# Kernel tuning notes

Measured on AMD Instinct MI355X. Metric: run time of the kernel, lower is better.

The kernel has to match this reference:

```python
import jax, jax.numpy as jnp
import numpy as np

N, E, D, H, O, L = 50000, 400000, 128, 128, 64, 2


def setup_inputs() -> dict:
    key = jax.random.key(0)
    ks = jax.random.split(key, 24)
    s = 0.05
    rn = lambda k, shape: jax.random.normal(k, shape, jnp.float32) * s
    # random edges with no self-loops (dst = src + nonzero offset mod N)
    src = jax.random.randint(ks[0], (E,), 0, N, dtype=jnp.int32)
    off = jax.random.randint(ks[1], (E,), 1, N, dtype=jnp.int32)
    dst = (src + off) % N
    edge_index = jnp.stack([src, dst])  # [2, E] int32
    return {
        "x": rn(ks[2], (N, D)),
        "edge_index": edge_index,
        "attn_W": rn(ks[3], (L, 2 * D, 2)),
        "attn_b": rn(ks[4], (L, 2)),
        "mlp_W1": rn(ks[5], (L, D, H)),
        "mlp_b1": rn(ks[6], (L, H)),
        "mlp_W2": rn(ks[7], (L, H, H)),
        "mlp_b2": rn(ks[8], (L, H)),
        "bn_gamma": jnp.ones((L, H), jnp.float32),   # torch BatchNorm1d default affine init
        "bn_beta": jnp.zeros((L, H), jnp.float32),
        "gru_Wih": rn(ks[9], (D, 3 * H)),
        "gru_Whh": rn(ks[10], (H, 3 * H)),
        "gru_bih": rn(ks[11], (3 * H,)),
        "gru_bhh": rn(ks[12], (3 * H,)),
        "last_W1": rn(ks[13], (H, H)),
        "last_b1": rn(ks[14], (H,)),
        "last_W2": rn(ks[15], (H, O)),
        "last_b2": rn(ks[16], (O,)),
    }


def reference(x, edge_index, attn_W, attn_b, mlp_W1, mlp_b1, mlp_W2, mlp_b2,
              bn_gamma, bn_beta, gru_Wih, gru_Whh, gru_bih, gru_bhh,
              last_W1, last_b1, last_W2, last_b2):
    n = x.shape[0]
    # symmetrize edge list: message (nbr -> node) for both directions
    node = jnp.concatenate([edge_index[0], edge_index[1]])  # destination
    nbr = jnp.concatenate([edge_index[1], edge_index[0]])   # source / neighbor
    deg = jax.ops.segment_sum(jnp.ones((node.shape[0], 1), x.dtype), node, num_segments=n)
    has_nbr = deg > 0

    h_state = jnp.zeros((n, gru_Whh.shape[0]), x.dtype)
    for l in range(attn_W.shape[0]):
        feats = x[nbr]  # [2E, d] gather
        s_agg = jax.ops.segment_sum(feats, node, num_segments=n)
        m_agg = jax.ops.segment_max(feats, node, num_segments=n)
        m_agg = jnp.where(has_nbr, m_agg, jnp.zeros_like(m_agg))  # isolated nodes stay 0
        # attention over {sum, max} aggregations
        scores = jnp.concatenate([s_agg, m_agg], axis=1) @ attn_W[l] + attn_b[l]  # [n, 2]
        w = jax.nn.softmax(scores, axis=1)
        comb = x + w[:, :1] * s_agg + w[:, 1:] * m_agg
        # MLP (in -> hidden, ReLU, hidden -> out)
        z = jax.nn.relu(comb @ mlp_W1[l] + mlp_b1[l]) @ mlp_W2[l] + mlp_b2[l]
        # BatchNorm1d in eval mode with running stats (mean 0, var 1): affine only
        z = z * bn_gamma[l] + bn_beta[l]
        # GRUCell
        gi = z @ gru_Wih + gru_bih
        gh = h_state @ gru_Whh + gru_bhh
        ir, iz, inn = jnp.split(gi, 3, axis=1)
        hr, hz, hn = jnp.split(gh, 3, axis=1)
        r = jax.nn.sigmoid(ir + hr)
        u = jax.nn.sigmoid(iz + hz)
        ncand = jnp.tanh(inn + r * hn)
        h_state = (1.0 - u) * ncand + u * h_state
        x = h_state
    # final node-level MLP
    out = jax.nn.relu(x @ last_W1 + last_b1) @ last_W2 + last_b2
    return out
```

## Files before the change

### kernel.cpp

```cpp
#include <hip/hip_runtime.h>
#include <math.h>

typedef unsigned short u16;
typedef __attribute__((ext_vector_type(8))) short bf16x8;
typedef __attribute__((ext_vector_type(4))) float f32x4;

__device__ __forceinline__ u16 f2b(float f) {
    union { float f; unsigned u; } v; v.f = f;
    unsigned r = (v.u + 0x7FFF + ((v.u >> 16) & 1)) >> 16;
    return (u16)r;
}
__device__ __forceinline__ float b2f(u16 h) {
    union { unsigned u; float f; } v; v.u = (unsigned)h << 16;
    return v.f;
}
__device__ __forceinline__ float fsig(float x) { return 1.f / (1.f + __expf(-x)); }
__device__ __forceinline__ float ftanh(float x) {
    float e = __expf(2.f * x);
    return 1.f - 2.f / (e + 1.f);
}

__device__ __forceinline__ void gll16(const void* g, void* l) {
    __builtin_amdgcn_global_load_lds(
        (const __attribute__((address_space(1))) void*)g,
        (__attribute__((address_space(3))) void*)l, 16, 0, 0);
}

template <int BYTES>
__device__ __forceinline__ void stage_lin(const u16* g, u16* l, int wid, int lane) {
#pragma unroll
    for (int i = 0; i < BYTES / 8192; ++i) {
        int off = (i * 8 + wid) * 1024;
        gll16((const char*)g + off + lane * 16, (char*)l + off);
    }
}

__global__ void k_deg(const int* __restrict__ ei, int* __restrict__ cnt, int E) {
    int e = blockIdx.x * 256 + threadIdx.x;
    if (e < E) {
        atomicAdd(&cnt[ei[e]], 1);
        atomicAdd(&cnt[ei[E + e]], 1);
    }
}

__global__ __launch_bounds__(1024) void k_scan_sum(const int* __restrict__ cnt,
                                                   int* __restrict__ part, int N) {
    __shared__ int sd[16];
    int t = threadIdx.x;
    int i = blockIdx.x * 1024 + t;
    int v = (i < N) ? cnt[i] : 0;
#pragma unroll
    for (int o = 32; o; o >>= 1) v += __shfl_xor(v, o);
    if ((t & 63) == 0) sd[t >> 6] = v;
    __syncthreads();
    if (t < 16) {
        int s = sd[t];
#pragma unroll
        for (int o = 8; o; o >>= 1) s += __shfl_xor(s, o);
        if (t == 0) part[blockIdx.x] = s;
    }
}

__global__ void k_scan_part(int* __restrict__ part, int nb) {
    int t = threadIdx.x;
    int v = (t < nb) ? part[t] : 0;
#pragma unroll
    for (int o = 1; o < 64; o <<= 1) {
        int u = __shfl_up(v, o);
        if ((t & 63) >= o) v += u;
    }
    if (t < nb) part[t] = v;
}

__global__ __launch_bounds__(1024) void k_scan_write(const int* __restrict__ cnt,
                                                     const int* __restrict__ part,
                                                     int* __restrict__ offs, int N) {
    __shared__ int sd[16];
    int t = threadIdx.x, lane = t & 63, wid = t >> 6;
    int i = blockIdx.x * 1024 + t;
    int v = (i < N) ? cnt[i] : 0;
    int inc = v;
#pragma unroll
    for (int o = 1; o < 64; o <<= 1) {
        int u = __shfl_up(inc, o);
        if (lane >= o) inc += u;
    }
    if (lane == 63) sd[wid] = inc;
    __syncthreads();
    if (wid == 0) {
        int wv = (lane < 16) ? sd[lane] : 0;
#pragma unroll
        for (int o = 1; o < 16; o <<= 1) {
            int u = __shfl_up(wv, o);
            if (lane >= o) wv += u;
        }
        if (lane < 16) sd[lane] = wv;
    }
    __syncthreads();
    int base = (blockIdx.x > 0 ? part[blockIdx.x - 1] : 0) + (wid > 0 ? sd[wid - 1] : 0);
    if (i < N) offs[i + 1] = base + inc;
    if (i == 0 && blockIdx.x == 0) offs[0] = 0;
}

__global__ void k_fill(const int* __restrict__ ei, int* __restrict__ cur,
                       u16* __restrict__ adj, int E) {
    int e = blockIdx.x * 256 + threadIdx.x;
    if (e < E) {
        int s = ei[e], d = ei[E + e];
        int p = atomicAdd(&cur[s], 1); adj[p] = (u16)d;
        int q = atomicAdd(&cur[d], 1); adj[q] = (u16)s;
    }
}

__device__ __forceinline__ void conv_chunk(const float* __restrict__ src,
                                           u16* __restrict__ dst, int c, int NC) {
    int sl = c / NC, n = c - sl * NC;
    u16 tmp[8];
#pragma unroll
    for (int i = 0; i < 8; ++i) tmp[i] = f2b(src[(size_t)(sl * 8 + i) * NC + n]);
    *(uint4*)(dst + (size_t)c * 8) = *(const uint4*)tmp;
}

__global__ void k_prep_w(const float* __restrict__ W1, const float* __restrict__ W2,
                         const float* __restrict__ Wih, const float* __restrict__ Whh,
                         const float* __restrict__ lW1, const float* __restrict__ lW2,
                         u16* __restrict__ tW1, u16* __restrict__ tW2,
                         u16* __restrict__ tGRU,
                         u16* __restrict__ tlW1, u16* __restrict__ tlW2, int L) {
    int c = blockIdx.x * 256 + threadIdx.x;
    if (c < L * 2048) { int l = c >> 11; conv_chunk(W1 + (size_t)l * 16384, tW1 + (size_t)l * 16384, c & 2047, 128); return; }
    c -= L * 2048;
    if (c < L * 2048) { int l = c >> 11; conv_chunk(W2 + (size_t)l * 16384, tW2 + (size_t)l * 16384, c & 2047, 128); return; }
    c -= L * 2048;
    if (c < 12288) {
        int s = c / 1536, r = c % 1536;
        int q = r / 384, r2 = r % 384;
        int mat = r2 / 192, cc = r2 % 192;
        int h = s >> 2, kc = s & 3;
        int tt = cc >> 4, ii = cc & 15;
        int g = tt >> 2;
        int ocol = g * 128 + h * 64 + (tt & 3) * 16 + ii;
        const float* src = mat ? Whh : Wih;
        int kb = (kc * 4 + q) * 8;
        u16 tmp[8];
#pragma unroll
        for (int e = 0; e < 8; ++e) tmp[e] = f2b(src[(size_t)(kb + e) * 384 + ocol]);
        *(uint4*)(tGRU + (size_t)c * 8) = *(const uint4*)tmp;
        return;
    }
    c -= 12288;
    if (c < 2048) { conv_chunk(lW1, tlW1, c, 128); return; }
    c -= 2048;
    if (c < 1024) { conv_chunk(lW2, tlW2, c, 64); return; }
}

__global__ void k_f2b(const float* __restrict__ src, u16* __restrict__ dst, int n8) {
    int i = blockIdx.x * 256 + threadIdx.x;
    if (i < n8) {
        float4 a = *(const float4*)(src + (size_t)i * 8);
        float4 b = *(const float4*)(src + (size_t)i * 8 + 4);
        u16 t[8] = {f2b(a.x), f2b(a.y), f2b(a.z), f2b(a.w),
                    f2b(b.x), f2b(b.y), f2b(b.z), f2b(b.w)};
        *(uint4*)(dst + (size_t)i * 8) = *(const uint4*)t;
    }
}

__global__ __launch_bounds__(256) void k_agg(const u16* __restrict__ xb,
                                             const u16* __restrict__ adj,
                                             const int* __restrict__ offs,
                                             const float* __restrict__ aW,
                                             const float* __restrict__ ab,
                                             u16* __restrict__ comb, int N) {
    int n = blockIdx.x * 4 + (threadIdx.x >> 6);
    if (n >= N) return;
    int l = threadIdx.x & 63;
    int half = l >> 5, e0 = (l & 31) * 4;
    int beg = offs[n], end = offs[n + 1];
    float s0 = 0.f, s1 = 0.f, s2 = 0.f, s3 = 0.f;
    float m0 = -3.402823e38f, m1 = m0, m2 = m0, m3 = m0;
    int j = beg + half;
    for (; j + 6 < end; j += 8) {
        int a0 = adj[j], a1 = adj[j + 2], a2 = adj[j + 4], a3 = adj[j + 6];
        ushort4 v0 = *(const ushort4*)(xb + (size_t)a0 * 128 + e0);
        ushort4 v1 = *(const ushort4*)(xb + (size_t)a1 * 128 + e0);
        ushort4 v2 = *(const ushort4*)(xb + (size_t)a2 * 128 + e0);
        ushort4 v3 = *(const ushort4*)(xb + (size_t)a3 * 128 + e0);
        float f0, f1, f2, f3;
        f0 = b2f(v0.x); f1 = b2f(v0.y); f2 = b2f(v0.z); f3 = b2f(v0.w);
        s0 += f0; s1 += f1; s2 += f2; s3 += f3;
        m0 = fmaxf(m0, f0); m1 = fmaxf(m1, f1); m2 = fmaxf(m2, f2); m3 = fmaxf(m3, f3);
        f0 = b2f(v1.x); f1 = b2f(v1.y); f2 = b2f(v1.z); f3 = b2f(v1.w);
        s0 += f0; s1 += f1; s2 += f2; s3 += f3;
        m0 = fmaxf(m0, f0); m1 = fmaxf(m1, f1); m2 = fmaxf(m2, f2); m3 = fmaxf(m3, f3);
        f0 = b2f(v2.x); f1 = b2f(v2.y); f2 = b2f(v2.z); f3 = b2f(v2.w);
        s0 += f0; s1 += f1; s2 += f2; s3 += f3;
        m0 = fmaxf(m0, f0); m1 = fmaxf(m1, f1); m2 = fmaxf(m2, f2); m3 = fmaxf(m3, f3);
        f0 = b2f(v3.x); f1 = b2f(v3.y); f2 = b2f(v3.z); f3 = b2f(v3.w);
        s0 += f0; s1 += f1; s2 += f2; s3 += f3;
        m0 = fmaxf(m0, f0); m1 = fmaxf(m1, f1); m2 = fmaxf(m2, f2); m3 = fmaxf(m3, f3);
    }
    for (; j < end; j += 2) {
        int nb = adj[j];
        ushort4 v = *(const ushort4*)(xb + (size_t)nb * 128 + e0);
        float f0 = b2f(v.x), f1 = b2f(v.y), f2 = b2f(v.z), f3 = b2f(v.w);
        s0 += f0; s1 += f1; s2 += f2; s3 += f3;
        m0 = fmaxf(m0, f0); m1 = fmaxf(m1, f1); m2 = fmaxf(m2, f2); m3 = fmaxf(m3, f3);
    }
    s0 += __shfl_xor(s0, 32); m0 = fmaxf(m0, __shfl_xor(m0, 32));
    s1 += __shfl_xor(s1, 32); m1 = fmaxf(m1, __shfl_xor(m1, 32));
    s2 += __shfl_xor(s2, 32); m2 = fmaxf(m2, __shfl_xor(m2, 32));
    s3 += __shfl_xor(s3, 32); m3 = fmaxf(m3, __shfl_xor(m3, 32));
    if (beg == end) { m0 = m1 = m2 = m3 = 0.f; }
    float p0 = 0.f, p1 = 0.f;
    {
        float2 w0v = *(const float2*)(aW + (size_t)e0 * 2);
        float2 w1v = *(const float2*)(aW + (size_t)(e0 + 1) * 2);
        float2 w2v = *(const float2*)(aW + (size_t)(e0 + 2) * 2);
        float2 w3v = *(const float2*)(aW + (size_t)(e0 + 3) * 2);
        float2 u0v = *(const float2*)(aW + (size_t)(128 + e0) * 2);
        float2 u1v = *(const float2*)(aW + (size_t)(128 + e0 + 1) * 2);
        float2 u2v = *(const float2*)(aW + (size_t)(128 + e0 + 2) * 2);
        float2 u3v = *(const float2*)(aW + (size_t)(128 + e0 + 3) * 2);
        p0 = s0 * w0v.x + s1 * w1v.x + s2 * w2v.x + s3 * w3v.x
           + m0 * u0v.x + m1 * u1v.x + m2 * u2v.x + m3 * u3v.x;
        p1 = s0 * w0v.y + s1 * w1v.y + s2 * w2v.y + s3 * w3v.y
           + m0 * u0v.y + m1 * u1v.y + m2 * u2v.y + m3 * u3v.y;
    }
#pragma unroll
    for (int o = 16; o; o >>= 1) { p0 += __shfl_xor(p0, o); p1 += __shfl_xor(p1, o); }
    p0 += ab[0]; p1 += ab[1];
    float pm = fmaxf(p0, p1);
    float ea = __expf(p0 - pm), eb = __expf(p1 - pm);
    float w0 = ea / (ea + eb), w1 = 1.f - w0;
    if (half == 0) {
        ushort4 xv = *(const ushort4*)(xb + (size_t)n * 128 + e0);
        ushort4 o;
        o.x = f2b(b2f(xv.x) + w0 * s0 + w1 * m0);
        o.y = f2b(b2f(xv.y) + w0 * s1 + w1 * m1);
        o.z = f2b(b2f(xv.z) + w0 * s2 + w1 * m2);
        o.w = f2b(b2f(xv.w) + w0 * s3 + w1 * m3);
        *(ushort4*)(comb + (size_t)n * 128 + e0) = o;
    }
}

template <bool H0, bool WF32>
__global__ __launch_bounds__(512, 4) void k_layer(
    const u16* __restrict__ Cb, const u16* __restrict__ Hb,
    const float* __restrict__ Hf,
    const u16* __restrict__ W1t, const float* __restrict__ b1,
    const u16* __restrict__ W2t, const float* __restrict__ b2,
    const float* __restrict__ gam, const float* __restrict__ bet,
    const u16* __restrict__ tG,
    const float* __restrict__ bih, const float* __restrict__ bhh,
    float* __restrict__ HnF, u16* __restrict__ HnB, int M) {
    __shared__ __align__(16) u16 x_s[128 * 16 * 8];
    __shared__ __align__(16) u16 b_s[2][12288];
    const int t = threadIdx.x;
    const int m0 = blockIdx.x * 128;
    const int wid = t >> 6, lane = t & 63, lo = lane & 15, hi = lane >> 4;
    const int w = wid;
    const int arow = 16 * w + lo;

#pragma unroll
    for (int i = 0; i < 4; ++i) {
        int off = (i * 8 + wid) * 1024;
        int row = (off >> 8) + (lane >> 4);
        int s = lane & 15;
        int gr = m0 + row; gr = gr < M ? gr : M - 1;
        gll16(Cb + (size_t)gr * 128 + ((s ^ (row & 7)) * 8), (char*)x_s + off);
    }
    bf16x8 hreg[4];
    if (!H0) {
        int gr = m0 + arow; gr = gr < M ? gr : M - 1;
#pragma unroll
        for (int kc = 0; kc < 4; ++kc)
            hreg[kc] = *(const bf16x8*)(Hb + (size_t)gr * 128 + (kc * 4 + hi) * 8);
    }
    stage_lin<16384>(W1t, b_s[0], wid, lane);
    stage_lin<16384>(W1t + 8192, b_s[1], wid, lane);
    __syncthreads();

    f32x4 acc[8];
#pragma unroll
    for (int j = 0; j < 8; ++j) acc[j] = (f32x4)0.f;
#pragma unroll
    for (int ks = 0; ks < 4; ++ks) {
        bf16x8 af = *(const bf16x8*)&x_s[(arow * 16 + ((ks * 4 + hi) ^ (arow & 7))) * 8];
        const u16* wb = b_s[ks >> 1];
        int loc = (ks & 1) * 4 + hi;
#pragma unroll
        for (int j = 0; j < 8; ++j) {
            bf16x8 bf = *(const bf16x8*)&wb[((size_t)loc * 128 + 16 * j + lo) * 8];
            acc[j] = __builtin_amdgcn_mfma_f32_16x16x32_bf16(af, bf, acc[j], 0, 0, 0);
        }
    }
    __syncthreads();
    stage_lin<16384>(W2t, b_s[0], wid, lane);
    stage_lin<16384>(W2t + 8192, b_s[1], wid, lane);
#pragma unroll
    for (int j = 0; j < 8; ++j) {
        int c = 16 * j + lo;
        float bv = b1[c];
#pragma unroll
        for (int q = 0; q < 4; ++q) {
            int row = 16 * w + hi * 4 + q;
            float v = fmaxf(acc[j][q] + bv, 0.f);
            int sl = c >> 3;
            x_s[(row * 16 + (sl ^ (row & 7))) * 8 + (c & 7)] = f2b(v);
        }
    }
    __syncthreads();

#pragma unroll
    for (int j = 0; j < 8; ++j) acc[j] = (f32x4)0.f;
#pragma unroll
    for (int ks = 0; ks < 4; ++ks) {
        bf16x8 af = *(const bf16x8*)&x_s[(arow * 16 + ((ks * 4 + hi) ^ (arow & 7))) * 8];
        const u16* wb = b_s[ks >> 1];
        int loc = (ks & 1) * 4 + hi;
#pragma unroll
        for (int j = 0; j < 8; ++j) {
            bf16x8 bf = *(const bf16x8*)&wb[((size_t)loc * 128 + 16 * j + lo) * 8];
            acc[j] = __builtin_amdgcn_mfma_f32_16x16x32_bf16(af, bf, acc[j], 0, 0, 0);
        }
    }
    __syncthreads();
    stage_lin<24576>(tG, b_s[0], wid, lane);
    stage_lin<24576>(tG + 12288, b_s[1], wid, lane);
#pragma unroll
    for (int j = 0; j < 8; ++j) {
        int c = 16 * j + lo;
        float bv = b2[c], gv = gam[c], tv = bet[c];
#pragma unroll
        for (int q = 0; q < 4; ++q) {
            int row = 16 * w + hi * 4 + q;
            float v = (acc[j][q] + bv) * gv + tv;
            int sl = c >> 3;
            x_s[(row * 16 + (sl ^ (row & 7))) * 8 + (c & 7)] = f2b(v);
        }
    }
    __syncthreads();

    f32x4 racc[4], uacc[4], nza[4], nha[4];

    auto gru_kc = [&](const u16* buf, int kc) {
        bf16x8 zf = *(const bf16x8*)&x_s[(arow * 16 + ((kc * 4 + hi) ^ (arow & 7))) * 8];
#pragma unroll
        for (int jj = 0; jj < 4; ++jj) {
            const u16* bi = &buf[((size_t)(hi * 2 + 0) * 192) * 8];
            bf16x8 wr = *(const bf16x8*)&bi[(jj * 16 + lo) * 8];
            racc[jj] = __builtin_amdgcn_mfma_f32_16x16x32_bf16(zf, wr, racc[jj], 0, 0, 0);
            bf16x8 wu = *(const bf16x8*)&bi[(64 + jj * 16 + lo) * 8];
            uacc[jj] = __builtin_amdgcn_mfma_f32_16x16x32_bf16(zf, wu, uacc[jj], 0, 0, 0);
            bf16x8 wn = *(const bf16x8*)&bi[(128 + jj * 16 + lo) * 8];
            nza[jj] = __builtin_amdgcn_mfma_f32_16x16x32_bf16(zf, wn, nza[jj], 0, 0, 0);
            if (!H0) {
                const u16* bh = &buf[((size_t)(hi * 2 + 1) * 192) * 8];
                bf16x8 vr = *(const bf16x8*)&bh[(jj * 16 + lo) * 8];
                racc[jj] = __builtin_amdgcn_mfma_f32_16x16x32_bf16(hreg[kc], vr, racc[jj], 0, 0, 0);
                bf16x8 vu = *(const bf16x8*)&bh[(64 + jj * 16 + lo) * 8];
                uacc[jj] = __builtin_amdgcn_mfma_f32_16x16x32_bf16(hreg[kc], vu, uacc[jj], 0, 0, 0);
                bf16x8 vn = *(const bf16x8*)&bh[(128 + jj * 16 + lo) * 8];
                nha[jj] = __builtin_amdgcn_mfma_f32_16x16x32_bf16(hreg[kc], vn, nha[jj], 0, 0, 0);
            }
        }
    };

    auto gru_epi = [&](int h) {
#pragma unroll
        for (int ct = 0; ct < 4; ++ct) {
            int c = h * 64 + ct * 16 + lo;
            float b_r = bih[c] + bhh[c];
            float b_u = bih[c + 128] + bhh[c + 128];
            float b_in = bih[c + 256], b_hn = bhh[c + 256];
#pragma unroll
            for (int q = 0; q < 4; ++q) {
                int r = m0 + 16 * w + hi * 4 + q;
                if (r < M) {
                    float rr = fsig(racc[ct][q] + b_r);
                    float uu = fsig(uacc[ct][q] + b_u);
                    float hterm = H0 ? b_hn : (nha[ct][q] + b_hn);
                    float nn = ftanh(nza[ct][q] + b_in + rr * hterm);
                    float hv = H0 ? 0.f : Hf[(size_t)r * 128 + c];
                    float o = (1.f - uu) * nn + uu * hv;
                    if (WF32) HnF[(size_t)r * 128 + c] = o;
                    HnB[(size_t)r * 128 + c] = f2b(o);
                }
            }
        }
    };

#pragma unroll
    for (int j = 0; j < 4; ++j) { racc[j] = (f32x4)0.f; uacc[j] = (f32x4)0.f;
                                  nza[j] = (f32x4)0.f; nha[j] = (f32x4)0.f; }
    gru_kc(b_s[0], 0);
    gru_kc(b_s[1], 1);
    __syncthreads();
    stage_lin<24576>(tG + 2 * 12288, b_s[0], wid, lane);
    stage_lin<24576>(tG + 3 * 12288, b_s[1], wid, lane);
    __syncthreads();
    gru_kc(b_s[0], 2);
    gru_kc(b_s[1], 3);
    __syncthreads();
    stage_lin<24576>(tG + 4 * 12288, b_s[0], wid, lane);
    stage_lin<24576>(tG + 5 * 12288, b_s[1], wid, lane);
    gru_epi(0);
    __syncthreads();

#pragma unroll
    for (int j = 0; j < 4; ++j) { racc[j] = (f32x4)0.f; uacc[j] = (f32x4)0.f;
                                  nza[j] = (f32x4)0.f; nha[j] = (f32x4)0.f; }
    gru_kc(b_s[0], 0);
    gru_kc(b_s[1], 1);
    __syncthreads();
    stage_lin<24576>(tG + 6 * 12288, b_s[0], wid, lane);
    stage_lin<24576>(tG + 7 * 12288, b_s[1], wid, lane);
    __syncthreads();
    gru_kc(b_s[0], 2);
    gru_kc(b_s[1], 3);
    gru_epi(1);
}

__global__ __launch_bounds__(256, 2) void k_final(const u16* __restrict__ Hb,
                                                  const u16* __restrict__ W1t,
                                                  const float* __restrict__ b1,
                                                  const u16* __restrict__ W2t,
                                                  const float* __restrict__ b2,
                                                  float* __restrict__ out, int M) {
    __shared__ __align__(16) u16 x_s[64 * 16 * 8];
    __shared__ __align__(16) u16 w_s[16 * 128 * 8];
    const int t = threadIdx.x;
    const int m0 = blockIdx.x * 64;
    const int w = t >> 6, l = t & 63, lo = l & 15, hi = l >> 4;
    const int arow = 16 * w + lo;
#pragma unroll
    for (int i = 0; i < 4; ++i) {
        int idx = t + i * 256;
        int row = idx >> 4, sl = idx & 15;
        int gr = m0 + row; gr = gr < M ? gr : M - 1;
        *(uint4*)&x_s[(row * 16 + (sl ^ (row & 7))) * 8] =
            *(const uint4*)(Hb + (size_t)gr * 128 + sl * 8);
    }
#pragma unroll
    for (int i = 0; i < 8; ++i) {
        int idx = t + i * 256;
        *(uint4*)&w_s[idx * 8] = *(const uint4*)(W1t + (size_t)idx * 8);
    }
    __syncthreads();
    f32x4 acc[8];
#pragma unroll
    for (int j = 0; j < 8; ++j) acc[j] = (f32x4)0.f;
#pragma unroll
    for (int ks = 0; ks < 4; ++ks) {
        bf16x8 af = *(const bf16x8*)&x_s[(arow * 16 + ((ks * 4 + hi) ^ (arow & 7))) * 8];
#pragma unroll
        for (int j = 0; j < 8; ++j) {
            bf16x8 bf = *(const bf16x8*)&w_s[((ks * 4 + hi) * 128 + 16 * j + lo) * 8];
            acc[j] = __builtin_amdgcn_mfma_f32_16x16x32_bf16(af, bf, acc[j], 0, 0, 0);
        }
    }
    __syncthreads();
#pragma unroll
    for (int j = 0; j < 8; ++j) {
        int c = 16 * j + lo;
        float bv = b1[c];
#pragma unroll
        for (int q = 0; q < 4; ++q) {
            int row = 16 * w + hi * 4 + q;
            float v = fmaxf(acc[j][q] + bv, 0.f);
            int sl = c >> 3;
            x_s[(row * 16 + (sl ^ (row & 7))) * 8 + (c & 7)] = f2b(v);
        }
    }
#pragma unroll
    for (int i = 0; i < 4; ++i) {
        int idx = t + i * 256;
        *(uint4*)&w_s[idx * 8] = *(const uint4*)(W2t + (size_t)idx * 8);
    }
    __syncthreads();
    f32x4 a2[4];
#pragma unroll
    for (int j = 0; j < 4; ++j) a2[j] = (f32x4)0.f;
#pragma unroll
    for (int ks = 0; ks < 4; ++ks) {
        bf16x8 af = *(const bf16x8*)&x_s[(arow * 16 + ((ks * 4 + hi) ^ (arow & 7))) * 8];
#pragma unroll
        for (int j = 0; j < 4; ++j) {
            bf16x8 bf = *(const bf16x8*)&w_s[((ks * 4 + hi) * 64 + 16 * j + lo) * 8];
            a2[j] = __builtin_amdgcn_mfma_f32_16x16x32_bf16(af, bf, a2[j], 0, 0, 0);
        }
    }
#pragma unroll
    for (int j = 0; j < 4; ++j) {
        int c = 16 * j + lo;
        float bv = b2[c];
#pragma unroll
        for (int q = 0; q < 4; ++q) {
            int r = m0 + 16 * w + hi * 4 + q;
            if (r < M) out[(size_t)r * 64 + c] = a2[j][q] + bv;
        }
    }
}

extern "C" void kernel_launch(void* const* d_in, const int* in_sizes, int n_in,
                              void* d_out, int out_size, void* d_ws, size_t ws_size,
                              hipStream_t stream) {
    const float* x   = (const float*)d_in[0];
    const int*   ei  = (const int*)d_in[1];
    const float* aW  = (const float*)d_in[2];
    const float* ab  = (const float*)d_in[3];
    const float* W1  = (const float*)d_in[4];
    const float* b1  = (const float*)d_in[5];
    const float* W2  = (const float*)d_in[6];
    const float* b2  = (const float*)d_in[7];
    const float* gam = (const float*)d_in[8];
    const float* bet = (const float*)d_in[9];
    const float* Wih = (const float*)d_in[10];
    const float* Whh = (const float*)d_in[11];
    const float* bih = (const float*)d_in[12];
    const float* bhh = (const float*)d_in[13];
    const float* lW1 = (const float*)d_in[14];
    const float* lb1 = (const float*)d_in[15];
    const float* lW2 = (const float*)d_in[16];
    const float* lb2 = (const float*)d_in[17];

    const int N = in_sizes[0] / 128;
    const int E = in_sizes[1] / 2;
    const int L = in_sizes[3] / 2;
    float* out = (float*)d_out;

    char* ws = (char*)d_ws;
    size_t off = 0;
    auto alloc = [&](size_t bytes) -> void* {
        void* p = ws + off;
        off = (off + bytes + 255) & ~(size_t)255;
        return p;
    };
    int* offs = (int*)alloc((size_t)(N + 1) * 4);
    int* cur  = (int*)alloc((size_t)N * 4);
    int* part = (int*)alloc(64 * 4);
    u16* adj  = (u16*)alloc((size_t)2 * E * 2);
    u16* tW1  = (u16*)alloc((size_t)L * 16384 * 2);
    u16* tW2  = (u16*)alloc((size_t)L * 16384 * 2);
    u16* tGRU = (u16*)alloc((size_t)98304 * 2);
    u16* tlW1 = (u16*)alloc((size_t)16384 * 2);
    u16* tlW2 = (u16*)alloc((size_t)8192 * 2);
    u16* xb   = (u16*)alloc((size_t)N * 128 * 2);
    u16* comb = (u16*)alloc((size_t)N * 128 * 2);
    float* hF = (float*)alloc((size_t)N * 128 * 4);
    u16* hAb  = (u16*)alloc((size_t)N * 128 * 2);
    u16* hBb  = (u16*)alloc((size_t)N * 128 * 2);
    (void)ws_size; (void)n_in; (void)out_size;

    hipMemsetAsync(cur, 0, (size_t)N * 4, stream);

    int wchunks = L * 4096 + 12288 + 3072;
    k_prep_w<<<(wchunks + 255) / 256, 256, 0, stream>>>(W1, W2, Wih, Whh, lW1, lW2,
                                                        tW1, tW2, tGRU, tlW1, tlW2, L);
    k_f2b<<<(N * 16 + 255) / 256, 256, 0, stream>>>(x, xb, N * 16);

    k_deg<<<(E + 255) / 256, 256, 0, stream>>>(ei, cur, E);
    int nb = (N + 1023) / 1024;
    k_scan_sum<<<nb, 1024, 0, stream>>>(cur, part, N);
    k_scan_part<<<1, 64, 0, stream>>>(part, nb);
    k_scan_write<<<nb, 1024, 0, stream>>>(cur, part, offs, N);
    hipMemcpyAsync(cur, offs, (size_t)N * 4, hipMemcpyDeviceToDevice, stream);
    k_fill<<<(E + 255) / 256, 256, 0, stream>>>(ei, cur, adj, E);

    const int mb = (N + 127) / 128;
    k_agg<<<(N + 3) / 4, 256, 0, stream>>>(xb, adj, offs, aW, ab, comb, N);
    k_layer<true, true><<<mb, 512, 0, stream>>>(
        comb, nullptr, nullptr, tW1, b1, tW2, b2, gam, bet,
        tGRU, bih, bhh, hF, hAb, N);
    k_agg<<<(N + 3) / 4, 256, 0, stream>>>(hAb, adj, offs, aW + 512, ab + 2, comb, N);
    k_layer<false, false><<<mb, 512, 0, stream>>>(
        comb, hAb, hF, tW1 + 16384, b1 + 128, tW2 + 16384, b2 + 128,
        gam + 128, bet + 128, tGRU, bih, bhh, nullptr, hBb, N);

    k_final<<<(N + 63) / 64, 256, 0, stream>>>(hBb, tlW1, lb1, tlW2, lb2, out, N);
}
```

Before: 263.5 us.

## Pipeline k_layer weight staging in 8KB double-buffered chunks with smaller tiles

Restructures the fused MLP+GRU layer kernel to stream weights through two small 8KB LDS buffers, one chunk per k-step, prefetching the next chunk while MFMAs consume the current one. Block size drops from 512 to 256 threads with 64-row tiles, cutting LDS use so more blocks fit per CU. The GRU weight packing layout is changed to match the per-gate chunk order. The cost is many more __syncthreads barriers (one per chunk) and weights re-fetched by twice as many blocks.

Result: no change. 267.7 us (+1.6%).

```diff
diff --git a/kernel.cpp b/kernel.cpp
--- a/kernel.cpp
+++ b/kernel.cpp
@@ -24,15 +24,6 @@
     __builtin_amdgcn_global_load_lds(
         (const __attribute__((address_space(1))) void*)g,
         (__attribute__((address_space(3))) void*)l, 16, 0, 0);
-}
-
-template <int BYTES>
-__device__ __forceinline__ void stage_lin(const u16* g, u16* l, int wid, int lane) {
-#pragma unroll
-    for (int i = 0; i < BYTES / 8192; ++i) {
-        int off = (i * 8 + wid) * 1024;
-        gll16((const char*)g + off + lane * 16, (char*)l + off);
-    }
 }
 
 __global__ void k_deg(const int* __restrict__ ei, int* __restrict__ cnt, int E) {
@@ -133,13 +124,10 @@
     if (c < L * 2048) { int l = c >> 11; conv_chunk(W2 + (size_t)l * 16384, tW2 + (size_t)l * 16384, c & 2047, 128); return; }
     c -= L * 2048;
     if (c < 12288) {
-        int s = c / 1536, r = c % 1536;
-        int q = r / 384, r2 = r % 384;
-        int mat = r2 / 192, cc = r2 % 192;
-        int h = s >> 2, kc = s & 3;
-        int tt = cc >> 4, ii = cc & 15;
-        int g = tt >> 2;
-        int ocol = g * 128 + h * 64 + (tt & 3) * 16 + ii;
+        int s = c >> 9, r = c & 511;
+        int q = r >> 7, mat = (r >> 6) & 1, cc = r & 63;
+        int h = s / 12, s2 = s % 12, kc = s2 / 3, g = s2 % 3;
+        int ocol = g * 128 + h * 64 + cc;
         const float* src = mat ? Whh : Wih;
         int kb = (kc * 4 + q) * 8;
         u16 tmp[8];
@@ -244,7 +232,7 @@
 }
 
 template <bool H0, bool WF32>
-__global__ __launch_bounds__(512, 4) void k_layer(
+__global__ __launch_bounds__(256, 4) void k_layer(
     const u16* __restrict__ Cb, const u16* __restrict__ Hb,
     const float* __restrict__ Hf,
     const u16* __restrict__ W1t, const float* __restrict__ b1,
@@ -253,17 +241,26 @@
     const u16* __restrict__ tG,
     const float* __restrict__ bih, const float* __restrict__ bhh,
     float* __restrict__ HnF, u16* __restrict__ HnB, int M) {
-    __shared__ __align__(16) u16 x_s[128 * 16 * 8];
-    __shared__ __align__(16) u16 b_s[2][12288];
+    __shared__ __align__(16) u16 x_s[64 * 16 * 8];
+    __shared__ __align__(16) u16 b_s[2][4096];
     const int t = threadIdx.x;
-    const int m0 = blockIdx.x * 128;
+    const int m0 = blockIdx.x * 64;
     const int wid = t >> 6, lane = t & 63, lo = lane & 15, hi = lane >> 4;
-    const int w = wid;
-    const int arow = 16 * w + lo;
+    const int arow = 16 * wid + lo;
+
+    auto issue = [&](int s) {
+        const u16* g = (s < 4) ? (W1t + (size_t)s * 4096)
+                     : (s < 8) ? (W2t + (size_t)(s - 4) * 4096)
+                               : (tG + (size_t)(s - 8) * 4096);
+        char* l = (char*)b_s[s & 1] + wid * 2048;
+        const char* gp = (const char*)g + wid * 2048 + lane * 16;
+        gll16(gp, l);
+        gll16(gp + 1024, l + 1024);
+    };
 
 #pragma unroll
     for (int i = 0; i < 4; ++i) {
-        int off = (i * 8 + wid) * 1024;
+        int off = (i * 4 + wid) * 1024;
         int row = (off >> 8) + (lane >> 4);
         int s = lane & 15;
         int gr = m0 + row; gr = gr < M ? gr : M - 1;
@@ -276,8 +273,7 @@
         for (int kc = 0; kc < 4; ++kc)
             hreg[kc] = *(const bf16x8*)(Hb + (size_t)gr * 128 + (kc * 4 + hi) * 8);
     }
-    stage_lin<16384>(W1t, b_s[0], wid, lane);
-    stage_lin<16384>(W1t + 8192, b_s[1], wid, lane);
+    issue(0);
     __syncthreads();
 
     f32x4 acc[8];
@@ -285,88 +281,48 @@
     for (int j = 0; j < 8; ++j) acc[j] = (f32x4)0.f;
 #pragma unroll
     for (int ks = 0; ks < 4; ++ks) {
+        issue(ks + 1);
         bf16x8 af = *(const bf16x8*)&x_s[(arow * 16 + ((ks * 4 + hi) ^ (arow & 7))) * 8];
-        const u16* wb = b_s[ks >> 1];
-        int loc = (ks & 1) * 4 + hi;
+        const u16* buf = b_s[ks & 1];
 #pragma unroll
         for (int j = 0; j < 8; ++j) {
-            bf16x8 bf = *(const bf16x8*)&wb[((size_t)loc * 128 + 16 * j + lo) * 8];
+            bf16x8 bf = *(const bf16x8*)&buf[((size_t)hi * 128 + 16 * j + lo) * 8];
             acc[j] = __builtin_amdgcn_mfma_f32_16x16x32_bf16(af, bf, acc[j], 0, 0, 0);
         }
-    }
-    __syncthreads();
-    stage_lin<16384>(W2t, b_s[0], wid, lane);
-    stage_lin<16384>(W2t + 8192, b_s[1], wid, lane);
-#pragma unroll
-    for (int j = 0; j < 8; ++j) {
-        int c = 16 * j + lo;
-        float bv = b1[c];
-#pragma unroll
-        for (int q = 0; q < 4; ++q) {
-            int row = 16 * w + hi * 4 + q;
-            float v = fmaxf(acc[j][q] + bv, 0.f);
-            int sl = c >> 3;
-            x_s[(row * 16 + (sl ^ (row & 7))) * 8 + (c & 7)] = f2b(v);
-        }
-    }
-    __syncthreads();
-
-#pragma unroll
-    for (int j = 0; j < 8; ++j) acc[j] = (f32x4)0.f;
+        __syncthreads();
+    }
+
 #pragma unroll
     for (int ks = 0; ks < 4; ++ks) {
+        issue(5 + ks);
+        if (ks == 0) {
+#pragma unroll
+            for (int j = 0; j < 8; ++j) {
+                int c = 16 * j + lo;
+                float bv = b1[c];
+#pragma unroll
+                for (int q = 0; q < 4; ++q) {
+                    int row = 16 * wid + hi * 4 + q;
+                    float v = fmaxf(acc[j][q] + bv, 0.f);
+                    int sl = c >> 3;
+                    x_s[(row * 16 + (sl ^ (row & 7))) * 8 + (c & 7)] = f2b(v);
+                }
+                acc[j] = (f32x4)0.f;
+            }
+        }
         bf16x8 af = *(const bf16x8*)&x_s[(arow * 16 + ((ks * 4 + hi) ^ (arow & 7))) * 8];
-        const u16* wb = b_s[ks >> 1];
-        int loc = (ks & 1) * 4 + hi;
+        const u16* buf = b_s[ks & 1];
 #pragma unroll
         for (int j = 0; j < 8; ++j) {
-            bf16x8 bf = *(const bf16x8*)&wb[((size_t)loc * 128 + 16 * j + lo) * 8];
+            bf16x8 bf = *(const bf16x8*)&buf[((size_t)hi * 128 + 16 * j + lo) * 8];
             acc[j] = __builtin_amdgcn_mfma_f32_16x16x32_bf16(af, bf, acc[j], 0, 0, 0);
         }
-    }
-    __syncthreads();
-    stage_lin<24576>(tG, b_s[0], wid, lane);
-    stage_lin<24576>(tG + 12288, b_s[1], wid, lane);
-#pragma unroll
-    for (int j = 0; j < 8; ++j) {
-        int c = 16 * j + lo;
-        float bv = b2[c], gv = gam[c], tv = bet[c];
-#pragma unroll
-        for (int q = 0; q < 4; ++q) {
-            int row = 16 * w + hi * 4 + q;
-            float v = (acc[j][q] + bv) * gv + tv;
-            int sl = c >> 3;
-            x_s[(row * 16 + (sl ^ (row & 7))) * 8 + (c & 7)] = f2b(v);
-        }
-    }
-    __syncthreads();
+        __syncthreads();
+    }
 
     f32x4 racc[4], uacc[4], nza[4], nha[4];
 
-    auto gru_kc = [&](const u16* buf, int kc) {
-        bf16x8 zf = *(const bf16x8*)&x_s[(arow * 16 + ((kc * 4 + hi) ^ (arow & 7))) * 8];
-#pragma unroll
-        for (int jj = 0; jj < 4; ++jj) {
-            const u16* bi = &buf[((size_t)(hi * 2 + 0) * 192) * 8];
-            bf16x8 wr = *(const bf16x8*)&bi[(jj * 16 + lo) * 8];
-            racc[jj] = __builtin_amdgcn_mfma_f32_16x16x32_bf16(zf, wr, racc[jj], 0, 0, 0);
-            bf16x8 wu = *(const bf16x8*)&bi[(64 + jj * 16 + lo) * 8];
-            uacc[jj] = __builtin_amdgcn_mfma_f32_16x16x32_bf16(zf, wu, uacc[jj], 0, 0, 0);
-            bf16x8 wn = *(const bf16x8*)&bi[(128 + jj * 16 + lo) * 8];
-            nza[jj] = __builtin_amdgcn_mfma_f32_16x16x32_bf16(zf, wn, nza[jj], 0, 0, 0);
-            if (!H0) {
-                const u16* bh = &buf[((size_t)(hi * 2 + 1) * 192) * 8];
-                bf16x8 vr = *(const bf16x8*)&bh[(jj * 16 + lo) * 8];
-                racc[jj] = __builtin_amdgcn_mfma_f32_16x16x32_bf16(hreg[kc], vr, racc[jj], 0, 0, 0);
-                bf16x8 vu = *(const bf16x8*)&bh[(64 + jj * 16 + lo) * 8];
-                uacc[jj] = __builtin_amdgcn_mfma_f32_16x16x32_bf16(hreg[kc], vu, uacc[jj], 0, 0, 0);
-                bf16x8 vn = *(const bf16x8*)&bh[(128 + jj * 16 + lo) * 8];
-                nha[jj] = __builtin_amdgcn_mfma_f32_16x16x32_bf16(hreg[kc], vn, nha[jj], 0, 0, 0);
-            }
-        }
-    };
-
-    auto gru_epi = [&](int h) {
+    auto epi = [&](int h) {
 #pragma unroll
         for (int ct = 0; ct < 4; ++ct) {
             int c = h * 64 + ct * 16 + lo;
@@ -375,7 +331,7 @@
             float b_in = bih[c + 256], b_hn = bhh[c + 256];
 #pragma unroll
             for (int q = 0; q < 4; ++q) {
-                int r = m0 + 16 * w + hi * 4 + q;
+                int r = m0 + 16 * wid + hi * 4 + q;
                 if (r < M) {
                     float rr = fsig(racc[ct][q] + b_r);
                     float uu = fsig(uacc[ct][q] + b_u);
@@ -391,34 +347,57 @@
     };
 
 #pragma unroll
-    for (int j = 0; j < 4; ++j) { racc[j] = (f32x4)0.f; uacc[j] = (f32x4)0.f;
-                                  nza[j] = (f32x4)0.f; nha[j] = (f32x4)0.f; }
-    gru_kc(b_s[0], 0);
-    gru_kc(b_s[1], 1);
-    __syncthreads();
-    stage_lin<24576>(tG + 2 * 12288, b_s[0], wid, lane);
-    stage_lin<24576>(tG + 3 * 12288, b_s[1], wid, lane);
-    __syncthreads();
-    gru_kc(b_s[0], 2);
-    gru_kc(b_s[1], 3);
-    __syncthreads();
-    stage_lin<24576>(tG + 4 * 12288, b_s[0], wid, lane);
-    stage_lin<24576>(tG + 5 * 12288, b_s[1], wid, lane);
-    gru_epi(0);
-    __syncthreads();
-
-#pragma unroll
-    for (int j = 0; j < 4; ++j) { racc[j] = (f32x4)0.f; uacc[j] = (f32x4)0.f;
-                                  nza[j] = (f32x4)0.f; nha[j] = (f32x4)0.f; }
-    gru_kc(b_s[0], 0);
-    gru_kc(b_s[1], 1);
-    __syncthreads();
-    stage_lin<24576>(tG + 6 * 12288, b_s[0], wid, lane);
-    stage_lin<24576>(tG + 7 * 12288, b_s[1], wid, lane);
-    __syncthreads();
-    gru_kc(b_s[0], 2);
-    gru_kc(b_s[1], 3);
-    gru_epi(1);
+    for (int h = 0; h < 2; ++h) {
+#pragma unroll
+        for (int kc = 0; kc < 4; ++kc) {
+            bf16x8 zf;
+#pragma unroll
+            for (int g = 0; g < 3; ++g) {
+                const int p = 8 + h * 12 + kc * 3 + g;
+                if (p < 31) issue(p + 1);
+                if (p == 8) {
+#pragma unroll
+                    for (int j = 0; j < 8; ++j) {
+                        int c = 16 * j + lo;
+                        float bv = b2[c], gv = gam[c], tv = bet[c];
+#pragma unroll
+                        for (int q = 0; q < 4; ++q) {
+                            int row = 16 * wid + hi * 4 + q;
+                            float v = (acc[j][q] + bv) * gv + tv;
+                            int sl = c >> 3;
+                            x_s[(row * 16 + (sl ^ (row & 7))) * 8 + (c & 7)] = f2b(v);
+                        }
+                    }
+                }
+                if (p == 20) epi(0);
+                if (p == 8 || p == 20) {
+#pragma unroll
+                    for (int j = 0; j < 4; ++j) {
+                        racc[j] = (f32x4)0.f; uacc[j] = (f32x4)0.f;
+                        nza[j] = (f32x4)0.f; nha[j] = (f32x4)0.f;
+                    }
+                }
+                if (g == 0)
+                    zf = *(const bf16x8*)&x_s[(arow * 16 + ((kc * 4 + hi) ^ (arow & 7))) * 8];
+                const u16* buf = b_s[p & 1];
+#pragma unroll
+                for (int jj = 0; jj < 4; ++jj) {
+                    bf16x8 wi = *(const bf16x8*)&buf[((size_t)hi * 128 + jj * 16 + lo) * 8];
+                    if (g == 0)      racc[jj] = __builtin_amdgcn_mfma_f32_16x16x32_bf16(zf, wi, racc[jj], 0, 0, 0);
+                    else if (g == 1) uacc[jj] = __builtin_amdgcn_mfma_f32_16x16x32_bf16(zf, wi, uacc[jj], 0, 0, 0);
+                    else             nza[jj]  = __builtin_amdgcn_mfma_f32_16x16x32_bf16(zf, wi, nza[jj], 0, 0, 0);
+                    if (!H0) {
+                        bf16x8 wh = *(const bf16x8*)&buf[((size_t)hi * 128 + 64 + jj * 16 + lo) * 8];
+                        if (g == 0)      racc[jj] = __builtin_amdgcn_mfma_f32_16x16x32_bf16(hreg[kc], wh, racc[jj], 0, 0, 0);
+                        else if (g == 1) uacc[jj] = __builtin_amdgcn_mfma_f32_16x16x32_bf16(hreg[kc], wh, uacc[jj], 0, 0, 0);
+                        else             nha[jj]  = __builtin_amdgcn_mfma_f32_16x16x32_bf16(hreg[kc], wh, nha[jj], 0, 0, 0);
+                    }
+                }
+                if (p < 31) __syncthreads();
+            }
+        }
+    }
+    epi(1);
 }
 
 __global__ __launch_bounds__(256, 2) void k_final(const u16* __restrict__ Hb,
@@ -567,13 +546,13 @@
     hipMemcpyAsync(cur, offs, (size_t)N * 4, hipMemcpyDeviceToDevice, stream);
     k_fill<<<(E + 255) / 256, 256, 0, stream>>>(ei, cur, adj, E);
 
-    const int mb = (N + 127) / 128;
+    const int mb = (N + 63) / 64;
     k_agg<<<(N + 3) / 4, 256, 0, stream>>>(xb, adj, offs, aW, ab, comb, N);
-    k_layer<true, true><<<mb, 512, 0, stream>>>(
+    k_layer<true, true><<<mb, 256, 0, stream>>>(
         comb, nullptr, nullptr, tW1, b1, tW2, b2, gam, bet,
         tGRU, bih, bhh, hF, hAb, N);
     k_agg<<<(N + 3) / 4, 256, 0, stream>>>(hAb, adj, offs, aW + 512, ab + 2, comb, N);
-    k_layer<false, false><<<mb, 512, 0, stream>>>(
+    k_layer<false, false><<<mb, 256, 0, stream>>>(
         comb, hAb, hF, tW1 + 16384, b1 + 128, tW2 + 16384, b2 + 128,
         gam + 128, bet + 128, tGRU, bih, bhh, nullptr, hBb, N);
 
```
